# Kernel optimization log

Measured on AMD Instinct MI355X. Metric: run time of the kernel, lower is better.

## Reference

```python
import jax, jax.numpy as jnp
import numpy as np

NB = 8      # n_blocks
DIM = 256   # model dim (= context_len in source)
DI = 512    # dim_inner = dim * expand(2)
DCONV = 4   # depthwise conv kernel
NS = 16     # d_state
DTR = 16    # dt_rank = ceil(dim/16)
NE = 4      # experts
INNER = 512 # MoE FFN inner = dim * multi(2)
L = 8192    # sequence length
HOR = 32    # horizon
EPS = 1e-3


def setup_inputs() -> dict:
    key = jax.random.key(0)
    ks = jax.random.split(key, 16)
    s = 0.02
    f = lambda k, shp: jax.random.normal(k, shp, jnp.float32) * s
    return {
        "x": jax.random.normal(ks[0], (DIM, L), jnp.float32),
        "lin_w": f(ks[1], (DIM, DIM)),                      # shared by self.linear and self.out (tied)
        "in_proj_w": f(ks[2], (NB, 2 * DI, DIM)),
        "conv_w": f(ks[3], (NB, DI, 1, DCONV)),             # depthwise conv, groups=DI
        "conv_b": f(ks[4], (NB, DI)),
        "x_proj_w": f(ks[5], (NB, DTR + 2 * NS, DI)),
        "dt_proj_w": f(ks[6], (NB, DI, DTR)),
        "dt_proj_b": f(ks[7], (NB, DI)),
        "A_log": jnp.tile(jnp.log(jnp.arange(1, NS + 1, dtype=jnp.float32)), (NB, DI, 1)),
        "D_param": jnp.ones((NB, DI), jnp.float32),
        "out_proj_w": f(ks[8], (NB, DIM, DI)),
        "gate_w": f(ks[9], (NB, NE, DIM)),
        "gproj_w": f(ks[10], (NB, NE, INNER, DIM)),
        "uproj_w": f(ks[11], (NB, NE, INNER, DIM)),
        "dproj_w": f(ks[12], (NB, NE, DIM, INNER)),
        "rms_a_w": jnp.ones((DIM,), jnp.float32),
        "rms_f_w": jnp.ones((DIM,), jnp.float32),
        "head_w1": f(ks[13], (DIM, DIM)),
        "head_w2": f(ks[14], (HOR, DIM)),
    }


def _rmsnorm(h, w):
    return w * (h * jax.lax.rsqrt(jnp.mean(h * h, axis=-1, keepdims=True) + EPS))


def _mamba(h, ipw, cw, cb, xpw, dtw, dtb, alog, dpar, opw):
    b = h.shape[0]
    xr = jnp.einsum('bld,od->bol', h, ipw)            # (b, 2*DI, l)
    xc, res = jnp.split(xr, 2, axis=1)                # each (b, DI, l)
    # causal depthwise conv (padding=DCONV-1, sliced to length l)
    xc = jax.lax.conv_general_dilated(xc, cw, (1,), [(DCONV - 1, 0)],
                                      feature_group_count=DI,
                                      dimension_numbers=('NCH', 'OIH', 'NCH'))
    xc = jax.nn.silu(xc + cb[None, :, None])
    A = -jnp.exp(alog)                                # (DI, NS)
    xdbl = jnp.einsum('bdl,kd->blk', xc, xpw)         # (b, l, DTR+2*NS)
    dr, B, C = xdbl[..., :DTR], xdbl[..., DTR:DTR + NS], xdbl[..., DTR + NS:]
    delta = jax.nn.softplus(jnp.einsum('blr,dr->bld', dr, dtw) + dtb)
    dA = jnp.exp(jnp.einsum('bld,dn->lbdn', delta, A))          # (l, b, DI, NS)
    dBu = jnp.einsum('bld,bln,bdl->lbdn', delta, B, xc)         # (l, b, DI, NS)
    Cl = jnp.transpose(C, (1, 0, 2))                             # (l, b, NS)
    def step(carry, inp):
        a, bu, c = inp
        carry = a * carry + bu
        return carry, jnp.einsum('bdn,bn->bd', carry, c)
    _, ys = jax.lax.scan(step, jnp.zeros((b, DI, NS), xc.dtype), (dA, dBu, Cl))
    y = jnp.transpose(ys, (1, 2, 0)) + xc * dpar[:, None]        # (b, DI, l)
    y = y * jax.nn.silu(res)
    return jnp.einsum('bdl,od->blo', y, opw)                     # (b, l, DIM)


def _moe(h, gw, gp, up, dp):
    shp = h.shape
    xf = h.reshape(-1, shp[-1])                       # (T, DIM)
    scores = xf @ gw.T                                # (T, NE)
    vals, idx = jax.lax.top_k(scores, 2)
    w = jax.nn.softmax(vals, axis=-1)                 # (T, 2)
    g = jax.nn.silu(jnp.einsum('td,ehd->teh', xf, gp))
    u = jnp.einsum('td,ehd->teh', xf, up)
    eo = jnp.einsum('teh,edh->ted', g * u, dp)        # (T, NE, DIM)
    we = jnp.sum(w[..., None] * jax.nn.one_hot(idx, NE, dtype=xf.dtype), axis=1)  # (T, NE)
    return jnp.einsum('te,ted->td', we, eo).reshape(shp)


def reference(x, lin_w, in_proj_w, conv_w, conv_b, x_proj_w, dt_proj_w, dt_proj_b,
              A_log, D_param, out_proj_w, gate_w, gproj_w, uproj_w, dproj_w,
              rms_a_w, rms_f_w, head_w1, head_w2):
    h = x.T[None]                                     # (1, L, DIM)
    h = h @ lin_w.T
    for i in range(NB):
        resi = h
        h = _rmsnorm(h, rms_a_w)
        h = _mamba(h, in_proj_w[i], conv_w[i], conv_b[i], x_proj_w[i],
                   dt_proj_w[i], dt_proj_b[i], A_log[i], D_param[i], out_proj_w[i])
        h = h + resi
        resi = h
        h = _moe(h, gate_w[i], gproj_w[i], uproj_w[i], dproj_w[i])
        h = _rmsnorm(h, rms_f_w)
        h = h + resi
    h = h @ lin_w.T                                   # self.out (tied weight)
    h = jax.nn.silu(h @ head_w1.T) @ head_w2.T        # head
    return jax.nn.sigmoid(h[0].T)                     # (HOR, L)
```

## Files before the change

kernel.cpp:

```cpp
#include <hip/hip_runtime.h>

typedef unsigned short u16;
typedef unsigned int u32;
using bf16x8 = __attribute__((ext_vector_type(8))) short;
using f32x4 = __attribute__((ext_vector_type(4))) float;

constexpr int kL = 8192;
constexpr int kDIM = 256;
constexpr int kDI = 512;
constexpr int kNB = 8;
constexpr float kEPS = 1e-3f;

__device__ __forceinline__ u16 f2b(float f) {
  u32 x = __builtin_bit_cast(u32, f);
  x += 0x7fffu + ((x >> 16) & 1u);
  return (u16)(x >> 16);
}
__device__ __forceinline__ float b2f(u16 u) {
  return __builtin_bit_cast(float, (u32)u << 16);
}
__device__ __forceinline__ float sigm(float x) { return 1.f / (1.f + __expf(-x)); }
__device__ __forceinline__ float softplus_fast(float x) {
  return fmaxf(x, 0.f) + __logf(1.f + __expf(-fabsf(x)));
}

__device__ __forceinline__ void async_cp16(const void* g, void* l) {
  __builtin_amdgcn_global_load_lds((const __attribute__((address_space(1))) u32*)g,
                                   (__attribute__((address_space(3))) u32*)l, 16, 0, 0);
}

struct Cvt2 {
  const float* s[23];
  u16* d[23];
  int n[23];
  int mode[23];
  int bstart[24];
  int nseg;
};
__global__ __launch_bounds__(256) void cvt2_k(Cvt2 dd) {
  const int b = blockIdx.x;
  int seg = 0;
  for (int i = 1; i < dd.nseg; ++i) seg += (b >= dd.bstart[i]) ? 1 : 0;
  const int lb = b - dd.bstart[seg];
  const float* s = dd.s[seg];
  u16* d = dd.d[seg];
  const int n = dd.n[seg];
  const int mode = dd.mode[seg];
  #pragma unroll
  for (int it = 0; it < 4; ++it) {
    const int e4 = lb * 1024 + it * 256 + threadIdx.x;
    const int i = e4 * 4;
    if (i >= n) break;
    const float4 v = ((const float4*)s)[e4];
    ushort4 o = make_ushort4(f2b(v.x), f2b(v.y), f2b(v.z), f2b(v.w));
    size_t dst;
    if (mode == 0) {
      dst = (size_t)i;
    } else if (mode == 1) {
      const int row = i >> 8, col = i & 255;
      const int drow = (row >> 9) * 1024 + ((row >> 4) & 31) * 32 + (row & 15);
      dst = (size_t)drow * 256 + col;
    } else {
      const int bb = i >> 19, e = (i >> 17) & 3, nr = (i >> 9) & 255, j = i & 511;
      dst = (size_t)bb * 524288 + (size_t)nr * 2048 + e * 512 + j;
    }
    *(ushort4*)&d[dst] = o;
  }
}

__global__ __launch_bounds__(256) void transpose_x_k(const float* __restrict__ x, u16* __restrict__ xT) {
  __shared__ float tile[32][33];
  int l0 = blockIdx.x * 32, d0 = blockIdx.y * 32;
  int tx = threadIdx.x, ty = threadIdx.y;
  #pragma unroll
  for (int i = 0; i < 32; i += 8)
    tile[ty + i][tx] = x[(size_t)(d0 + ty + i) * kL + l0 + tx];
  __syncthreads();
  #pragma unroll
  for (int i = 0; i < 32; i += 8)
    xT[(size_t)(l0 + ty + i) * kDIM + d0 + tx] = f2b(tile[tx][ty + i]);
}

template <int BM, int BN, int TR, int TC, int WCN, int MODE>
__global__ __launch_bounds__(256) void gemm_t(
    const u16* __restrict__ A, int lda,
    const u16* __restrict__ W, int ldw,
    void* __restrict__ C, int ldc,
    int N, int K, int pstride)
{
  constexpr int BNR = (BN + 63) & ~63;
  constexpr int NA = BM * 64 / 2048;
  constexpr int NBt = BNR * 64 / 2048;
  __shared__ u16 As[BM * 64];
  __shared__ u16 Bs[BNR * 64];
  const int tid = threadIdx.x;
  const int lane = tid & 63;
  const int wave = tid >> 6;
  const int bm = blockIdx.x * BM;
  const int bn = blockIdx.y * BN;
  const int wrow = (wave / WCN) * (TR * 16);
  const int wcol = (wave % WCN) * (TC * 16);
  const int kchunk = K / (int)gridDim.z;
  const int kbeg = blockIdx.z * kchunk;
  const int niter = kchunk >> 6;

  const u16* aSrc[NA];
  int aDst[NA];
  #pragma unroll
  for (int it = 0; it < NA; ++it) {
    const int flat = (it * 256 + tid) * 8;
    const int r = flat >> 6;
    const int gc = ((((flat >> 3) & 7) ^ (r & 7)) << 3);
    aDst[it] = flat;
    aSrc[it] = A + (size_t)(bm + r) * lda + kbeg + gc;
  }
  const u16* bSrc[NBt];
  int bDst[NBt];
  #pragma unroll
  for (int it = 0; it < NBt; ++it) {
    const int flat = (it * 256 + tid) * 8;
    const int r = flat >> 6;
    const int gc = ((((flat >> 3) & 7) ^ (r & 7)) << 3);
    int n = bn + r;
    if (n > N - 1) n = N - 1;
    bDst[it] = flat;
    bSrc[it] = W + (size_t)n * ldw + kbeg + gc;
  }

  f32x4 acc[TR][TC];
  #pragma unroll
  for (int r = 0; r < TR; ++r)
    #pragma unroll
    for (int c = 0; c < TC; ++c)
      acc[r][c] = f32x4{0.f, 0.f, 0.f, 0.f};

  for (int ki = 0; ki < niter; ++ki) {
    #pragma unroll
    for (int it = 0; it < NA; ++it) {
      async_cp16(aSrc[it], &As[aDst[it]]);
      aSrc[it] += 64;
    }
    #pragma unroll
    for (int it = 0; it < NBt; ++it) {
      async_cp16(bSrc[it], &Bs[bDst[it]]);
      bSrc[it] += 64;
    }
    __syncthreads();
    #pragma unroll
    for (int kk = 0; kk < 64; kk += 32) {
      const int kc = (kk >> 3) + (lane >> 4);
      const int mrow = lane & 15;
      bf16x8 a[TR], b[TC];
      #pragma unroll
      for (int rr = 0; rr < TR; ++rr) {
        int row = wrow + rr * 16 + mrow;
        a[rr] = *(const bf16x8*)&As[row * 64 + ((kc ^ (row & 7)) << 3)];
      }
      #pragma unroll
      for (int cc = 0; cc < TC; ++cc) {
        int row = wcol + cc * 16 + mrow;
        b[cc] = *(const bf16x8*)&Bs[row * 64 + ((kc ^ (row & 7)) << 3)];
      }
      #pragma unroll
      for (int rr = 0; rr < TR; ++rr)
        #pragma unroll
        for (int cc = 0; cc < TC; ++cc)
          acc[rr][cc] = __builtin_amdgcn_mfma_f32_16x16x32_bf16(a[rr], b[cc], acc[rr][cc], 0, 0, 0);
    }
    __syncthreads();
  }

  const int colb = bn + wcol + (lane & 15);
  const int rowb = bm + wrow + ((lane >> 4) << 2);
  #pragma unroll
  for (int rr = 0; rr < TR; ++rr)
    #pragma unroll
    for (int cc = 0; cc < TC; ++cc) {
      int col = colb + cc * 16;
      if (col >= N) continue;
      #pragma unroll
      for (int i = 0; i < 4; ++i) {
        const int row = rowb + rr * 16 + i;
        size_t off = (size_t)row * ldc + col;
        float v = acc[rr][cc][i];
        if constexpr (MODE == 0) ((float*)C)[off] = v;
        else if constexpr (MODE == 2) ((u16*)C)[off] = f2b(v);
        else if constexpr (MODE == 3) ((u16*)C)[off] = f2b(v * sigm(v));
        else if constexpr (MODE == 4) atomicAdd(&((float*)C)[off], v);
        else if constexpr (MODE == 5) ((float*)C)[off + (size_t)blockIdx.z * pstride] = v;
        else if constexpr (MODE == 7) ((float*)C)[(size_t)col * kL + row] = sigm(v);
      }
    }
}

__global__ __launch_bounds__(512, 1) void moe_mega_k(
    float* __restrict__ h, const float* __restrict__ hpart,
    const float* __restrict__ gw,
    const u16* __restrict__ Wgu, const u16* __restrict__ Wd,
    const float* __restrict__ wf, const float* __restrict__ wa,
    u16* __restrict__ hb2, u16* __restrict__ hn)
{
  __shared__ u16 Ah[32 * 256];
  __shared__ u16 Ts[32 * 512];
  __shared__ u16 Ws[2][256 * 64];
  __shared__ float WeS[32][4];
  const int tid = threadIdx.x;
  const int lane = tid & 63;
  const int quad = lane >> 4;
  const int m16 = lane & 15;
  const int wave = tid >> 6;
  const int wcol = wave * 32;
  const int r0 = blockIdx.x * 32;
  const int prow = tid >> 4;
  const int pcol = (tid & 15) * 16;

  float hv[16];
  {
    const size_t base = (size_t)(r0 + prow) * 256 + pcol;
    #pragma unroll
    for (int j = 0; j < 16; j += 4) {
      float4 v = *(const float4*)(h + base + j);
      #pragma unroll
      for (int z = 0; z < 2; ++z) {
        const float4 pv = *(const float4*)(hpart + (size_t)z * 2097152 + base + j);
        v.x += pv.x; v.y += pv.y; v.z += pv.z; v.w += pv.w;
      }
      hv[j] = v.x; hv[j + 1] = v.y; hv[j + 2] = v.z; hv[j + 3] = v.w;
    }
  }
  {
    float p[4];
    #pragma unroll
    for (int e = 0; e < 4; ++e) {
      float s = 0.f;
      #pragma unroll
      for (int j = 0; j < 16; ++j) s += hv[j] * gw[e * 256 + pcol + j];
      p[e] = s;
    }
    #pragma unroll
    for (int o = 8; o > 0; o >>= 1) {
      p[0] += __shfl_xor(p[0], o); p[1] += __shfl_xor(p[1], o);
      p[2] += __shfl_xor(p[2], o); p[3] += __shfl_xor(p[3], o);
    }
    if ((tid & 15) == 0) {
      int i0 = 0;
      #pragma unroll
      for (int e = 1; e < 4; ++e) if (p[e] > p[i0]) i0 = e;
      int i1 = -1;
      #pragma unroll
      for (int e = 0; e < 4; ++e) {
        if (e == i0) continue;
        if (i1 < 0 || p[e] > p[i1]) i1 = e;
      }
      const float tt = __expf(p[i1] - p[i0]);
      float o0 = 1.f / (1.f + tt), o1 = tt / (1.f + tt);
      WeS[prow][0] = 0.f; WeS[prow][1] = 0.f; WeS[prow][2] = 0.f; WeS[prow][3] = 0.f;
      WeS[prow][i0] = o0; WeS[prow][i1] = o1;
    }
    #pragma unroll
    for (int cc = 0; cc < 2; ++cc) {
      const int chunk = (pcol >> 3) + cc;
      const int sw = ((chunk ^ (prow & 7)) << 3);
      u16 tmp[8];
      #pragma unroll
      for (int j = 0; j < 8; ++j) tmp[j] = f2b(hv[cc * 8 + j]);
      *(bf16x8*)&Ah[prow * 256 + sw] = *(bf16x8*)tmp;
    }
  }
  __syncthreads();

  f32x4 macc[2][2];
  #pragma unroll
  for (int rt = 0; rt < 2; ++rt)
    #pragma unroll
    for (int ct = 0; ct < 2; ++ct) macc[rt][ct] = f32x4{0.f, 0.f, 0.f, 0.f};

  auto stage_gu = [&](int buf, int e, int nc, int k0) {
    #pragma unroll
    for (int it = 0; it < 4; ++it) {
      const int flat = (it * 512 + tid) * 8;
      const int r = flat >> 6;
      const int gc = ((((flat >> 3) & 7) ^ (r & 7)) << 3);
      async_cp16(Wgu + (size_t)(e * 1024 + nc * 256 + r) * 256 + k0 + gc, &Ws[buf][flat]);
    }
  };
  auto stage_dp = [&](int buf, int e, int k0) {
    #pragma unroll
    for (int it = 0; it < 4; ++it) {
      const int flat = (it * 512 + tid) * 8;
      const int r = flat >> 6;
      const int gc = ((((flat >> 3) & 7) ^ (r & 7)) << 3);
      async_cp16(Wd + (size_t)r * 2048 + e * 512 + k0 + gc, &Ws[buf][flat]);
    }
  };

  for (int e = 0; e < 4; ++e) {
    for (int nc = 0; nc < 4; ++nc) {
      f32x4 acc[2][2];
      #pragma unroll
      for (int rt = 0; rt < 2; ++rt)
        #pragma unroll
        for (int ct = 0; ct < 2; ++ct) acc[rt][ct] = f32x4{0.f, 0.f, 0.f, 0.f};
      stage_gu(0, e, nc, 0);
      __syncthreads();
      #pragma unroll
      for (int k0i = 0; k0i < 4; ++k0i) {
        if (k0i < 3) stage_gu((k0i + 1) & 1, e, nc, (k0i + 1) * 64);
        const u16* buf = Ws[k0i & 1];
        #pragma unroll
        for (int kk = 0; kk < 64; kk += 32) {
          const int kcs = (kk >> 3) + quad;
          bf16x8 a[2], b[2];
          #pragma unroll
          for (int rt = 0; rt < 2; ++rt) {
            const int row = rt * 16 + m16;
            const int ch = ((k0i * 64 + kk) >> 3) + quad;
            a[rt] = *(const bf16x8*)&Ah[row * 256 + ((ch ^ (row & 7)) << 3)];
          }
          #pragma unroll
          for (int ct = 0; ct < 2; ++ct) {
            const int n = wcol + ct * 16 + m16;
            b[ct] = *(const bf16x8*)&buf[n * 64 + ((kcs ^ (n & 7)) << 3)];
          }
          #pragma unroll
          for (int rt = 0; rt < 2; ++rt)
            #pragma unroll
            for (int ct = 0; ct < 2; ++ct)
              acc[rt][ct] = __builtin_amdgcn_mfma_f32_16x16x32_bf16(a[rt], b[ct], acc[rt][ct], 0, 0, 0);
        }
        __syncthreads();
      }
      const int group = nc * 8 + wave;
      const int j = group * 16 + m16;
      #pragma unroll
      for (int rt = 0; rt < 2; ++rt)
        #pragma unroll
        for (int i = 0; i < 4; ++i) {
          const int row = rt * 16 + quad * 4 + i;
          const float g = acc[rt][0][i];
          const float u = acc[rt][1][i];
          const float val = g * sigm(g) * u * WeS[row][e];
          Ts[row * 512 + (((j >> 3) ^ (row & 7)) << 3) + (j & 7)] = f2b(val);
        }
    }
    __syncthreads();
    stage_dp(0, e, 0);
    __syncthreads();
    #pragma unroll
    for (int k0i = 0; k0i < 8; ++k0i) {
      if (k0i < 7) stage_dp((k0i + 1) & 1, e, (k0i + 1) * 64);
      const u16* buf = Ws[k0i & 1];
      #pragma unroll
      for (int kk = 0; kk < 64; kk += 32) {
        const int kcs = (kk >> 3) + quad;
        bf16x8 a[2], b[2];
        #pragma unroll
        for (int rt = 0; rt < 2; ++rt) {
          const int row = rt * 16 + m16;
          const int ch = ((k0i * 64 + kk) >> 3) + quad;
          a[rt] = *(const bf16x8*)&Ts[row * 512 + ((ch ^ (row & 7)) << 3)];
        }
        #pragma unroll
        for (int ct = 0; ct < 2; ++ct) {
          const int n = wcol + ct * 16 + m16;
          b[ct] = *(const bf16x8*)&buf[n * 64 + ((kcs ^ (n & 7)) << 3)];
        }
        #pragma unroll
        for (int rt = 0; rt < 2; ++rt)
          #pragma unroll
          for (int ct = 0; ct < 2; ++ct)
            macc[rt][ct] = __builtin_amdgcn_mfma_f32_16x16x32_bf16(a[rt], b[ct], macc[rt][ct], 0, 0, 0);
      }
      __syncthreads();
    }
  }

  float* MoeS = (float*)Ts;
  __syncthreads();
  #pragma unroll
  for (int rt = 0; rt < 2; ++rt)
    #pragma unroll
    for (int ct = 0; ct < 2; ++ct)
      #pragma unroll
      for (int i = 0; i < 4; ++i)
        MoeS[(rt * 16 + quad * 4 + i) * 256 + wcol + ct * 16 + m16] = macc[rt][ct][i];
  __syncthreads();

  float mv[16];
  float ss = 0.f;
  #pragma unroll
  for (int j = 0; j < 16; ++j) {
    mv[j] = MoeS[prow * 256 + pcol + j];
    ss += mv[j] * mv[j];
  }
  #pragma unroll
  for (int o = 8; o > 0; o >>= 1) ss += __shfl_xor(ss, o);
  const float r1 = rsqrtf(ss * (1.f / 256.f) + kEPS);
  float ss2 = 0.f;
  #pragma unroll
  for (int j = 0; j < 16; ++j) {
    hv[j] += wf[pcol + j] * mv[j] * r1;
    ss2 += hv[j] * hv[j];
  }
  #pragma unroll
  for (int o = 8; o > 0; o >>= 1) ss2 += __shfl_xor(ss2, o);
  const float r2 = rsqrtf(ss2 * (1.f / 256.f) + kEPS);

  const size_t base = (size_t)(r0 + prow) * 256 + pcol;
  #pragma unroll
  for (int j = 0; j < 16; j += 4)
    *(float4*)(h + base + j) = float4{hv[j], hv[j + 1], hv[j + 2], hv[j + 3]};
  #pragma unroll
  for (int j = 0; j < 16; j += 4) {
    *(ushort4*)(hb2 + base + j) = make_ushort4(f2b(hv[j]), f2b(hv[j + 1]), f2b(hv[j + 2]), f2b(hv[j + 3]));
    *(ushort4*)(hn + base + j) = make_ushort4(
        f2b(wa[pcol + j] * hv[j] * r2), f2b(wa[pcol + j + 1] * hv[j + 1] * r2),
        f2b(wa[pcol + j + 2] * hv[j + 2] * r2), f2b(wa[pcol + j + 3] * hv[j + 3] * r2));
  }
}

__device__ __forceinline__ float block_sum256(float v) {
  #pragma unroll
  for (int o = 32; o > 0; o >>= 1) v += __shfl_down(v, o);
  __shared__ float red[4];
  __syncthreads();
  if ((threadIdx.x & 63) == 0) red[threadIdx.x >> 6] = v;
  __syncthreads();
  return red[0] + red[1] + red[2] + red[3];
}

__global__ __launch_bounds__(256) void rms_a_k(const float* __restrict__ h, const float* __restrict__ w,
                                               u16* __restrict__ hn) {
  const int l = blockIdx.x, t = threadIdx.x;
  const float v = h[(size_t)l * kDIM + t];
  const float ssum = block_sum256(v * v);
  const float r = rsqrtf(ssum * (1.f / 256.f) + kEPS);
  hn[(size_t)l * kDIM + t] = f2b(w[t] * v * r);
}

__global__ __launch_bounds__(256) void conv_silu_k(const u16* __restrict__ xz, const float* __restrict__ cw,
                                                   const float* __restrict__ cb,
                                                   u16* __restrict__ xcb, u16* __restrict__ zsb,
                                                   float* __restrict__ xdbl) {
  const int i4 = blockIdx.x * 256 + threadIdx.x;
  if (i4 < 98304) *(float4*)&xdbl[i4 * 4] = float4{0.f, 0.f, 0.f, 0.f};
  const int l = i4 >> 7;
  const int d = (i4 & 127) * 4;
  float acc[4];
  const float4 cbv = *(const float4*)&cb[d];
  acc[0] = cbv.x; acc[1] = cbv.y; acc[2] = cbv.z; acc[3] = cbv.w;
  #pragma unroll
  for (int j = 0; j < 4; ++j) {
    const int ll = l - 3 + j;
    if (ll >= 0) {
      const ushort4 xv = *(const ushort4*)&xz[(size_t)ll * 1024 + d];
      acc[0] += cw[(d + 0) * 4 + j] * b2f(xv.x);
      acc[1] += cw[(d + 1) * 4 + j] * b2f(xv.y);
      acc[2] += cw[(d + 2) * 4 + j] * b2f(xv.z);
      acc[3] += cw[(d + 3) * 4 + j] * b2f(xv.w);
    }
  }
  ushort4 xo, zo;
  const ushort4 zv = *(const ushort4*)&xz[(size_t)l * 1024 + 512 + d];
  float z0 = b2f(zv.x), z1 = b2f(zv.y), z2 = b2f(zv.z), z3 = b2f(zv.w);
  xo.x = f2b(acc[0] * sigm(acc[0])); xo.y = f2b(acc[1] * sigm(acc[1]));
  xo.z = f2b(acc[2] * sigm(acc[2])); xo.w = f2b(acc[3] * sigm(acc[3]));
  zo.x = f2b(z0 * sigm(z0)); zo.y = f2b(z1 * sigm(z1));
  zo.z = f2b(z2 * sigm(z2)); zo.w = f2b(z3 * sigm(z3));
  *(ushort4*)&xcb[(size_t)l * 512 + d] = xo;
  *(ushort4*)&zsb[(size_t)l * 512 + d] = zo;
}

__global__ __launch_bounds__(256) void scan_a_k(const float* __restrict__ xdbl, const u16* __restrict__ xcb,
                                                const float* __restrict__ A_log, const float* __restrict__ dtw,
                                                const float* __restrict__ dtb,
                                                u16* __restrict__ delta,
                                                float* __restrict__ aprod, float* __restrict__ bacc) {
  const int c = blockIdx.x;
  const int t = threadIdx.x;
  const int half = t & 1;
  const int d = blockIdx.y * 128 + (t >> 1);
  const int l0 = c * 64;
  __shared__ float Xs[64][32];
  for (int i = t; i < 2048; i += 256)
    Xs[i >> 5][i & 31] = xdbl[(size_t)(l0 + (i >> 5)) * 48 + (i & 31)];
  __syncthreads();
  float wd[8], Ad[8];
  #pragma unroll
  for (int j = 0; j < 8; ++j) wd[j] = dtw[d * 16 + half * 8 + j];
  const float bd = dtb[d];
  #pragma unroll
  for (int n = 0; n < 8; ++n) Ad[n] = -__expf(A_log[d * 16 + half * 8 + n]);
  float s[8], ap[8];
  #pragma unroll
  for (int n = 0; n < 8; ++n) { s[n] = 0.f; ap[n] = 1.f; }
  #pragma unroll 4
  for (int lr = 0; lr < 64; ++lr) {
    const float4 dr0 = *(const float4*)&Xs[lr][half * 8];
    const float4 dr1 = *(const float4*)&Xs[lr][half * 8 + 4];
    float p0 = dr0.x * wd[0] + dr0.y * wd[1] + dr0.z * wd[2] + dr0.w * wd[3];
    float p1 = dr1.x * wd[4] + dr1.y * wd[5] + dr1.z * wd[6] + dr1.w * wd[7];
    float dot = p0 + p1;
    dot += __shfl_xor(dot, 1);
    const float dl = softplus_fast(dot + bd);
    const int l = l0 + lr;
    if (!half) delta[(size_t)l * 512 + d] = f2b(dl);
    const float du = dl * b2f(xcb[(size_t)l * 512 + d]);
    const float4 B0 = *(const float4*)&Xs[lr][16 + half * 8];
    const float4 B1 = *(const float4*)&Xs[lr][16 + half * 8 + 4];
    const float Bv[8] = {B0.x, B0.y, B0.z, B0.w, B1.x, B1.y, B1.z, B1.w};
    #pragma unroll
    for (int n = 0; n < 8; ++n) {
      const float a = __expf(dl * Ad[n]);
      s[n] = fmaf(a, s[n], du * Bv[n]);
      ap[n] *= a;
    }
  }
  const int base = c * 8192 + d * 16 + half * 8;
  #pragma unroll
  for (int n = 0; n < 8; ++n) { aprod[base + n] = ap[n]; bacc[base + n] = s[n]; }
}

__global__ __launch_bounds__(256) void scan_b1_k(const float* __restrict__ aprod, const float* __restrict__ bacc,
                                                 float* __restrict__ gp, float* __restrict__ gb) {
  const int idx = blockIdx.x * 256 + threadIdx.x;
  const int st = idx & 8191, g = idx >> 13;
  float P = 1.f, S = 0.f;
  #pragma unroll
  for (int k = 0; k < 8; ++k) {
    const int c = g * 8 + k;
    const float a = aprod[(size_t)c * 8192 + st];
    S = fmaf(a, S, bacc[(size_t)c * 8192 + st]);
    P *= a;
  }
  gp[(size_t)g * 8192 + st] = P;
  gb[(size_t)g * 8192 + st] = S;
}

__global__ __launch_bounds__(256) void scan_b2_k(const float* __restrict__ gp, const float* __restrict__ gb,
                                                 float* __restrict__ ginit) {
  const int st = blockIdx.x * 256 + threadIdx.x;
  float cur = 0.f;
  #pragma unroll
  for (int g = 0; g < 16; ++g) {
    ginit[(size_t)g * 8192 + st] = cur;
    cur = fmaf(gp[(size_t)g * 8192 + st], cur, gb[(size_t)g * 8192 + st]);
  }
}

__global__ __launch_bounds__(256) void scan_b3_k(const float* __restrict__ aprod, const float* __restrict__ bacc,
                                                 const float* __restrict__ ginit, float* __restrict__ sinit) {
  const int idx = blockIdx.x * 256 + threadIdx.x;
  const int st = idx & 8191, g = idx >> 13;
  float cur = ginit[(size_t)g * 8192 + st];
  #pragma unroll
  for (int k = 0; k < 8; ++k) {
    const int c = g * 8 + k;
    sinit[(size_t)c * 8192 + st] = cur;
    cur = fmaf(aprod[(size_t)c * 8192 + st], cur, bacc[(size_t)c * 8192 + st]);
  }
}

__global__ __launch_bounds__(256) void scan_c_k(const float* __restrict__ xdbl, const u16* __restrict__ xcb,
                                                const u16* __restrict__ zsb, const float* __restrict__ A_log,
                                                const u16* __restrict__ delta,
                                                const float* __restrict__ sinit,
                                                const float* __restrict__ Dp, u16* __restrict__ yv) {
  const int c = blockIdx.x;
  const int t = threadIdx.x;
  const int half = t & 1;
  const int d = blockIdx.y * 128 + (t >> 1);
  const int l0 = c * 64;
  __shared__ float Xs[64][32];
  for (int i = t; i < 2048; i += 256)
    Xs[i >> 5][i & 31] = xdbl[(size_t)(l0 + (i >> 5)) * 48 + 16 + (i & 31)];
  __syncthreads();
  float Ad[8];
  #pragma unroll
  for (int n = 0; n < 8; ++n) Ad[n] = -__expf(A_log[d * 16 + half * 8 + n]);
  float s[8];
  const int base = c * 8192 + d * 16 + half * 8;
  #pragma unroll
  for (int n = 0; n < 8; ++n) s[n] = sinit[base + n];
  const float Dd = Dp[d];
  #pragma unroll 4
  for (int lr = 0; lr < 64; ++lr) {
    const int l = l0 + lr;
    const float dl = b2f(delta[(size_t)l * 512 + d]);
    const float xv = b2f(xcb[(size_t)l * 512 + d]);
    const float zs = b2f(zsb[(size_t)l * 512 + d]);
    const float du = dl * xv;
    const float4 B0 = *(const float4*)&Xs[lr][half * 8];
    const float4 B1 = *(const float4*)&Xs[lr][half * 8 + 4];
    const float4 C0 = *(const float4*)&Xs[lr][16 + half * 8];
    const float4 C1 = *(const float4*)&Xs[lr][16 + half * 8 + 4];
    const float Bv[8] = {B0.x, B0.y, B0.z, B0.w, B1.x, B1.y, B1.z, B1.w};
    const float Cv[8] = {C0.x, C0.y, C0.z, C0.w, C1.x, C1.y, C1.z, C1.w};
    float y = 0.f;
    #pragma unroll
    for (int n = 0; n < 8; ++n) {
      const float a = __expf(dl * Ad[n]);
      s[n] = fmaf(a, s[n], du * Bv[n]);
      y = fmaf(s[n], Cv[n], y);
    }
    y += __shfl_xor(y, 1);
    if (!half) yv[(size_t)l * 512 + d] = f2b((y + xv * Dd) * zs);
  }
}

extern "C" void kernel_launch(void* const* d_in, const int* in_sizes, int n_in,
                              void* d_out, int out_size, void* d_ws, size_t ws_size,
                              hipStream_t stream) {
  const float* x        = (const float*)d_in[0];
  const float* lin_w    = (const float*)d_in[1];
  const float* in_proj  = (const float*)d_in[2];
  const float* conv_w   = (const float*)d_in[3];
  const float* conv_b   = (const float*)d_in[4];
  const float* x_proj   = (const float*)d_in[5];
  const float* dt_w     = (const float*)d_in[6];
  const float* dt_b     = (const float*)d_in[7];
  const float* A_log    = (const float*)d_in[8];
  const float* D_param  = (const float*)d_in[9];
  const float* out_proj = (const float*)d_in[10];
  const float* gate_w   = (const float*)d_in[11];
  const float* gproj    = (const float*)d_in[12];
  const float* uproj    = (const float*)d_in[13];
  const float* dproj    = (const float*)d_in[14];
  const float* rms_a_w  = (const float*)d_in[15];
  const float* rms_f_w  = (const float*)d_in[16];
  const float* head_w1  = (const float*)d_in[17];
  const float* head_w2  = (const float*)d_in[18];

  char* p = (char*)d_ws;
  auto alloc = [&](size_t bytes) -> char* {
    char* r = p;
    p += (bytes + 255) & ~(size_t)255;
    return r;
  };

  u16* lin_b  = (u16*)alloc(65536 * 2);
  u16* ipw_b  = (u16*)alloc((size_t)2097152 * 2);
  u16* xpw_b  = (u16*)alloc((size_t)196608 * 2);
  u16* opw_b  = (u16*)alloc((size_t)1048576 * 2);
  u16* gupw_b = (u16*)alloc((size_t)8388608 * 2);
  u16* dpw_b  = (u16*)alloc((size_t)4194304 * 2);
  u16* hw1_b  = (u16*)alloc(65536 * 2);
  u16* hw2_b  = (u16*)alloc(8192 * 2);

  u16* xT     = (u16*)alloc((size_t)kL * kDIM * 2);
  float* h    = (float*)alloc((size_t)kL * kDIM * 4);
  u16* hn     = (u16*)alloc((size_t)kL * kDIM * 2);
  u16* hb2    = (u16*)alloc((size_t)kL * kDIM * 2);
  float* xdbl = (float*)alloc((size_t)kL * 48 * 4);
  u16* fb     = (u16*)alloc((size_t)kL * kDIM * 2);
  u16* h2b    = (u16*)alloc((size_t)kL * kDIM * 2);
  u16* xz     = (u16*)alloc((size_t)kL * 1024 * 2);
  u16* xcb    = (u16*)alloc((size_t)kL * kDI * 2);
  u16* zsb    = (u16*)alloc((size_t)kL * kDI * 2);
  u16* yv     = (u16*)alloc((size_t)kL * kDI * 2);
  u16* delta  = (u16*)alloc((size_t)kL * kDI * 2);
  float* aprod = (float*)alloc((size_t)128 * 8192 * 4);
  float* bacc  = (float*)alloc((size_t)128 * 8192 * 4);
  float* sinit = (float*)alloc((size_t)128 * 8192 * 4);
  float* gp    = (float*)alloc((size_t)16 * 8192 * 4);
  float* gb    = (float*)alloc((size_t)16 * 8192 * 4);
  float* ginit = (float*)alloc((size_t)16 * 8192 * 4);
  float* hpart = (float*)alloc((size_t)2 * kL * kDIM * 4);

  if ((size_t)(p - (char*)d_ws) > ws_size) return;

  Cvt2 dd;
  int seg = 0, blk = 0;
  auto add = [&](const float* s, u16* d, int n, int mode) {
    dd.s[seg] = s; dd.d[seg] = d; dd.n[seg] = n; dd.mode[seg] = mode;
    dd.bstart[seg] = blk;
    blk += (n + 4095) / 4096;
    ++seg;
  };
  add(lin_w, lin_b, 65536, 0);
  add(in_proj, ipw_b, 2097152, 0);
  add(x_proj, xpw_b, 196608, 0);
  add(out_proj, opw_b, 1048576, 0);
  add(head_w1, hw1_b, 65536, 0);
  add(head_w2, hw2_b, 8192, 0);
  for (int i = 0; i < kNB; ++i) {
    add(gproj + (size_t)i * 524288, gupw_b + (size_t)i * 1048576, 524288, 1);
    add(uproj + (size_t)i * 524288, gupw_b + (size_t)i * 1048576 + 4096, 524288, 1);
  }
  add(dproj, dpw_b, 4194304, 2);
  dd.nseg = seg;
  dd.bstart[seg] = blk;
  cvt2_k<<<blk, 256, 0, stream>>>(dd);
  transpose_x_k<<<dim3(kL / 32, kDIM / 32), dim3(32, 8), 0, stream>>>(x, xT);

  gemm_t<64, 128, 2, 4, 2, 0><<<dim3(128, 2, 1), 256, 0, stream>>>(
      xT, 256, lin_b, 256, h, 256, 256, 256, 0);
  rms_a_k<<<kL, 256, 0, stream>>>(h, rms_a_w, hn);

  for (int i = 0; i < kNB; ++i) {
    gemm_t<128, 128, 4, 4, 2, 2><<<dim3(64, 8, 1), 256, 0, stream>>>(
        hn, 256, ipw_b + (size_t)i * 262144, 256, xz, 1024, 1024, 256, 0);
    conv_silu_k<<<kL * kDI / 1024, 256, 0, stream>>>(xz, conv_w + (size_t)i * 2048,
                                                     conv_b + (size_t)i * 512, xcb, zsb, xdbl);
    gemm_t<128, 48, 2, 3, 1, 4><<<dim3(64, 1, 8), 256, 0, stream>>>(
        xcb, 512, xpw_b + (size_t)i * 24576, 512, xdbl, 48, 48, 512, 0);
    scan_a_k<<<dim3(128, 4), 256, 0, stream>>>(xdbl, xcb, A_log + (size_t)i * 8192,
                                               dt_w + (size_t)i * 8192, dt_b + (size_t)i * 512,
                                               delta, aprod, bacc);
    scan_b1_k<<<512, 256, 0, stream>>>(aprod, bacc, gp, gb);
    scan_b2_k<<<32, 256, 0, stream>>>(gp, gb, ginit);
    scan_b3_k<<<512, 256, 0, stream>>>(aprod, bacc, ginit, sinit);
    scan_c_k<<<dim3(128, 4), 256, 0, stream>>>(xdbl, xcb, zsb, A_log + (size_t)i * 8192,
                                               delta, sinit, D_param + (size_t)i * 512, yv);
    gemm_t<128, 128, 4, 4, 2, 5><<<dim3(64, 2, 2), 256, 0, stream>>>(
        yv, 512, opw_b + (size_t)i * 131072, 512, hpart, 256, 256, 512, 2097152);
    moe_mega_k<<<256, 512, 0, stream>>>(h, hpart, gate_w + (size_t)i * 1024,
                                        gupw_b + (size_t)i * 1048576, dpw_b + (size_t)i * 524288,
                                        rms_f_w, rms_a_w, hb2, hn);
  }

  gemm_t<64, 128, 2, 4, 2, 2><<<dim3(128, 2, 1), 256, 0, stream>>>(
      hb2, 256, lin_b, 256, h2b, 256, 256, 256, 0);
  gemm_t<64, 128, 2, 4, 2, 3><<<dim3(128, 2, 1), 256, 0, stream>>>(
      h2b, 256, hw1_b, 256, fb, 256, 256, 256, 0);
  gemm_t<64, 128, 2, 4, 2, 7><<<dim3(128, 1, 1), 256, 0, stream>>>(
      fb, 256, hw2_b, 256, (float*)d_out, 32, 32, 256, 0);
}
```

Before: 2.008 ms.

## Fuse out_proj GEMM into MoE kernel and fold scan_b3 into scan_c

The out_proj GEMM (yv x Wop), which previously wrote split-K partials to a float buffer, is now computed inside moe_mega_k per 32-row tile, with the result staged in shared memory and added to the residual. The scan_b3 kernel that materialised per-chunk initial states is removed; scan_c now derives its initial state from ginit by replaying up to 7 chunk aprod/bacc products. This removes two launches per block and the hpart/sinit global round-trips. In exchange each MoE block performs more serial work, and the out_proj now runs on only 256 blocks without split-K.

Result: no change. 1.994 ms (-0.7%).

```diff
diff --git a/kernel.cpp b/kernel.cpp
--- a/kernel.cpp
+++ b/kernel.cpp
@@ -187,14 +187,13 @@
         else if constexpr (MODE == 2) ((u16*)C)[off] = f2b(v);
         else if constexpr (MODE == 3) ((u16*)C)[off] = f2b(v * sigm(v));
         else if constexpr (MODE == 4) atomicAdd(&((float*)C)[off], v);
-        else if constexpr (MODE == 5) ((float*)C)[off + (size_t)blockIdx.z * pstride] = v;
         else if constexpr (MODE == 7) ((float*)C)[(size_t)col * kL + row] = sigm(v);
       }
     }
 }
 
 __global__ __launch_bounds__(512, 1) void moe_mega_k(
-    float* __restrict__ h, const float* __restrict__ hpart,
+    float* __restrict__ h, const u16* __restrict__ yv, const u16* __restrict__ Wop,
     const float* __restrict__ gw,
     const u16* __restrict__ Wgu, const u16* __restrict__ Wd,
     const float* __restrict__ wf, const float* __restrict__ wa,
@@ -214,18 +213,96 @@
   const int prow = tid >> 4;
   const int pcol = (tid & 15) * 16;
 
+  auto stage_op = [&](int buf, int k0) {
+    #pragma unroll
+    for (int it = 0; it < 4; ++it) {
+      const int flat = (it * 512 + tid) * 8;
+      const int r = flat >> 6;
+      const int gc = ((((flat >> 3) & 7) ^ (r & 7)) << 3);
+      async_cp16(Wop + (size_t)r * 512 + k0 + gc, &Ws[buf][flat]);
+    }
+  };
+  auto stage_gu = [&](int buf, int e, int nc, int k0) {
+    #pragma unroll
+    for (int it = 0; it < 4; ++it) {
+      const int flat = (it * 512 + tid) * 8;
+      const int r = flat >> 6;
+      const int gc = ((((flat >> 3) & 7) ^ (r & 7)) << 3);
+      async_cp16(Wgu + (size_t)(e * 1024 + nc * 256 + r) * 256 + k0 + gc, &Ws[buf][flat]);
+    }
+  };
+  auto stage_dp = [&](int buf, int e, int k0) {
+    #pragma unroll
+    for (int it = 0; it < 4; ++it) {
+      const int flat = (it * 512 + tid) * 8;
+      const int r = flat >> 6;
+      const int gc = ((((flat >> 3) & 7) ^ (r & 7)) << 3);
+      async_cp16(Wd + (size_t)r * 2048 + e * 512 + k0 + gc, &Ws[buf][flat]);
+    }
+  };
+
+  #pragma unroll
+  for (int it = 0; it < 4; ++it) {
+    const int flat = (it * 512 + tid) * 8;
+    const int row = flat >> 9;
+    const int c = (flat >> 3) & 63;
+    const int cs = (c & ~7) | ((c & 7) ^ (row & 7));
+    async_cp16(yv + (size_t)(r0 + row) * 512 + cs * 8, &Ts[flat]);
+  }
+  f32x4 hacc[2][2];
+  #pragma unroll
+  for (int rt = 0; rt < 2; ++rt)
+    #pragma unroll
+    for (int ct = 0; ct < 2; ++ct) hacc[rt][ct] = f32x4{0.f, 0.f, 0.f, 0.f};
+  stage_op(0, 0);
+  __syncthreads();
+  #pragma unroll
+  for (int k0i = 0; k0i < 8; ++k0i) {
+    if (k0i < 7) stage_op((k0i + 1) & 1, (k0i + 1) * 64);
+    const u16* buf = Ws[k0i & 1];
+    #pragma unroll
+    for (int kk = 0; kk < 64; kk += 32) {
+      const int kcs = (kk >> 3) + quad;
+      bf16x8 a[2], b[2];
+      #pragma unroll
+      for (int rt = 0; rt < 2; ++rt) {
+        const int row = rt * 16 + m16;
+        const int ch = ((k0i * 64 + kk) >> 3) + quad;
+        a[rt] = *(const bf16x8*)&Ts[row * 512 + ((ch ^ (row & 7)) << 3)];
+      }
+      #pragma unroll
+      for (int ct = 0; ct < 2; ++ct) {
+        const int n = wcol + ct * 16 + m16;
+        b[ct] = *(const bf16x8*)&buf[n * 64 + ((kcs ^ (n & 7)) << 3)];
+      }
+      #pragma unroll
+      for (int rt = 0; rt < 2; ++rt)
+        #pragma unroll
+        for (int ct = 0; ct < 2; ++ct)
+          hacc[rt][ct] = __builtin_amdgcn_mfma_f32_16x16x32_bf16(a[rt], b[ct], hacc[rt][ct], 0, 0, 0);
+    }
+    __syncthreads();
+  }
+  float* MoeS = (float*)Ts;
+  #pragma unroll
+  for (int rt = 0; rt < 2; ++rt)
+    #pragma unroll
+    for (int ct = 0; ct < 2; ++ct)
+      #pragma unroll
+      for (int i = 0; i < 4; ++i)
+        MoeS[(rt * 16 + quad * 4 + i) * 256 + wcol + ct * 16 + m16] = hacc[rt][ct][i];
+  __syncthreads();
+
   float hv[16];
   {
     const size_t base = (size_t)(r0 + prow) * 256 + pcol;
     #pragma unroll
     for (int j = 0; j < 16; j += 4) {
-      float4 v = *(const float4*)(h + base + j);
-      #pragma unroll
-      for (int z = 0; z < 2; ++z) {
-        const float4 pv = *(const float4*)(hpart + (size_t)z * 2097152 + base + j);
-        v.x += pv.x; v.y += pv.y; v.z += pv.z; v.w += pv.w;
-      }
-      hv[j] = v.x; hv[j + 1] = v.y; hv[j + 2] = v.z; hv[j + 3] = v.w;
+      const float4 v = *(const float4*)(h + base + j);
+      hv[j] = v.x + MoeS[prow * 256 + pcol + j];
+      hv[j + 1] = v.y + MoeS[prow * 256 + pcol + j + 1];
+      hv[j + 2] = v.z + MoeS[prow * 256 + pcol + j + 2];
+      hv[j + 3] = v.w + MoeS[prow * 256 + pcol + j + 3];
     }
   }
   {
@@ -274,25 +351,6 @@
   for (int rt = 0; rt < 2; ++rt)
     #pragma unroll
     for (int ct = 0; ct < 2; ++ct) macc[rt][ct] = f32x4{0.f, 0.f, 0.f, 0.f};
-
-  auto stage_gu = [&](int buf, int e, int nc, int k0) {
-    #pragma unroll
-    for (int it = 0; it < 4; ++it) {
-      const int flat = (it * 512 + tid) * 8;
-      const int r = flat >> 6;
-      const int gc = ((((flat >> 3) & 7) ^ (r & 7)) << 3);
-      async_cp16(Wgu + (size_t)(e * 1024 + nc * 256 + r) * 256 + k0 + gc, &Ws[buf][flat]);
-    }
-  };
-  auto stage_dp = [&](int buf, int e, int k0) {
-    #pragma unroll
-    for (int it = 0; it < 4; ++it) {
-      const int flat = (it * 512 + tid) * 8;
-      const int r = flat >> 6;
-      const int gc = ((((flat >> 3) & 7) ^ (r & 7)) << 3);
-      async_cp16(Wd + (size_t)r * 2048 + e * 512 + k0 + gc, &Ws[buf][flat]);
-    }
-  };
 
   for (int e = 0; e < 4; ++e) {
     for (int nc = 0; nc < 4; ++nc) {
@@ -375,8 +433,6 @@
     }
   }
 
-  float* MoeS = (float*)Ts;
-  __syncthreads();
   #pragma unroll
   for (int rt = 0; rt < 2; ++rt)
     #pragma unroll
@@ -548,23 +604,11 @@
   }
 }
 
-__global__ __launch_bounds__(256) void scan_b3_k(const float* __restrict__ aprod, const float* __restrict__ bacc,
-                                                 const float* __restrict__ ginit, float* __restrict__ sinit) {
-  const int idx = blockIdx.x * 256 + threadIdx.x;
-  const int st = idx & 8191, g = idx >> 13;
-  float cur = ginit[(size_t)g * 8192 + st];
-  #pragma unroll
-  for (int k = 0; k < 8; ++k) {
-    const int c = g * 8 + k;
-    sinit[(size_t)c * 8192 + st] = cur;
-    cur = fmaf(aprod[(size_t)c * 8192 + st], cur, bacc[(size_t)c * 8192 + st]);
-  }
-}
-
 __global__ __launch_bounds__(256) void scan_c_k(const float* __restrict__ xdbl, const u16* __restrict__ xcb,
                                                 const u16* __restrict__ zsb, const float* __restrict__ A_log,
                                                 const u16* __restrict__ delta,
-                                                const float* __restrict__ sinit,
+                                                const float* __restrict__ aprod, const float* __restrict__ bacc,
+                                                const float* __restrict__ ginit,
                                                 const float* __restrict__ Dp, u16* __restrict__ yv) {
   const int c = blockIdx.x;
   const int t = threadIdx.x;
@@ -579,9 +623,24 @@
   #pragma unroll
   for (int n = 0; n < 8; ++n) Ad[n] = -__expf(A_log[d * 16 + half * 8 + n]);
   float s[8];
-  const int base = c * 8192 + d * 16 + half * 8;
-  #pragma unroll
-  for (int n = 0; n < 8; ++n) s[n] = sinit[base + n];
+  {
+    const int g = c >> 3;
+    const int stb = d * 16 + half * 8;
+    const float4 g0 = *(const float4*)&ginit[(size_t)g * 8192 + stb];
+    const float4 g1 = *(const float4*)&ginit[(size_t)g * 8192 + stb + 4];
+    s[0] = g0.x; s[1] = g0.y; s[2] = g0.z; s[3] = g0.w;
+    s[4] = g1.x; s[5] = g1.y; s[6] = g1.z; s[7] = g1.w;
+    for (int cc = g * 8; cc < c; ++cc) {
+      const float4 a0 = *(const float4*)&aprod[(size_t)cc * 8192 + stb];
+      const float4 a1 = *(const float4*)&aprod[(size_t)cc * 8192 + stb + 4];
+      const float4 b0 = *(const float4*)&bacc[(size_t)cc * 8192 + stb];
+      const float4 b1 = *(const float4*)&bacc[(size_t)cc * 8192 + stb + 4];
+      s[0] = fmaf(a0.x, s[0], b0.x); s[1] = fmaf(a0.y, s[1], b0.y);
+      s[2] = fmaf(a0.z, s[2], b0.z); s[3] = fmaf(a0.w, s[3], b0.w);
+      s[4] = fmaf(a1.x, s[4], b1.x); s[5] = fmaf(a1.y, s[5], b1.y);
+      s[6] = fmaf(a1.z, s[6], b1.z); s[7] = fmaf(a1.w, s[7], b1.w);
+    }
+  }
   const float Dd = Dp[d];
   #pragma unroll 4
   for (int lr = 0; lr < 64; ++lr) {
@@ -661,11 +720,9 @@
   u16* delta  = (u16*)alloc((size_t)kL * kDI * 2);
   float* aprod = (float*)alloc((size_t)128 * 8192 * 4);
   float* bacc  = (float*)alloc((size_t)128 * 8192 * 4);
-  float* sinit = (float*)alloc((size_t)128 * 8192 * 4);
   float* gp    = (float*)alloc((size_t)16 * 8192 * 4);
   float* gb    = (float*)alloc((size_t)16 * 8192 * 4);
   float* ginit = (float*)alloc((size_t)16 * 8192 * 4);
-  float* hpart = (float*)alloc((size_t)2 * kL * kDIM * 4);
 
   if ((size_t)(p - (char*)d_ws) > ws_size) return;
 
@@ -709,12 +766,11 @@
                                                delta, aprod, bacc);
     scan_b1_k<<<512, 256, 0, stream>>>(aprod, bacc, gp, gb);
     scan_b2_k<<<32, 256, 0, stream>>>(gp, gb, ginit);
-    scan_b3_k<<<512, 256, 0, stream>>>(aprod, bacc, ginit, sinit);
     scan_c_k<<<dim3(128, 4), 256, 0, stream>>>(xdbl, xcb, zsb, A_log + (size_t)i * 8192,
-                                               delta, sinit, D_param + (size_t)i * 512, yv);
-    gemm_t<128, 128, 4, 4, 2, 5><<<dim3(64, 2, 2), 256, 0, stream>>>(
-        yv, 512, opw_b + (size_t)i * 131072, 512, hpart, 256, 256, 512, 2097152);
-    moe_mega_k<<<256, 512, 0, stream>>>(h, hpart, gate_w + (size_t)i * 1024,
+                                               delta, aprod, bacc, ginit,
+                                               D_param + (size_t)i * 512, yv);
+    moe_mega_k<<<256, 512, 0, stream>>>(h, yv, opw_b + (size_t)i * 131072,
+                                        gate_w + (size_t)i * 1024,
                                         gupw_b + (size_t)i * 1048576, dpw_b + (size_t)i * 524288,
                                         rms_f_w, rms_a_w, hb2, hn);
   }
```
